# Optimization experiments

Measured on AMD Instinct MI355X. Metric: run time of the kernel, lower is better.

Reference implementation:

```python
import jax, jax.numpy as jnp
import numpy as np

B, N = 8, 64          # batch, keywords per utterance
D = 768               # audio/transformer d_model
T = 512               # CLIP text embedding dim
V = 49408             # CLIP BPE vocab size
TAU = 0.1             # VQ softmax temperature
EPS = 1e-8            # cosine-similarity eps (matches F.cosine_similarity)


def setup_inputs() -> dict:
    key = jax.random.key(0)
    k1, k2, k3 = jax.random.split(key, 3)
    return {
        "audio_feat": jax.random.normal(k1, (B, N, D), dtype=jnp.float32),
        "W_proj": jax.random.normal(k2, (D, T), dtype=jnp.float32) * 0.02,
        "b_proj": jnp.zeros((T,), dtype=jnp.float32),
        "token_emb": jax.random.normal(k3, (V, T), dtype=jnp.float32) * 0.02,
    }


def _l2_normalize(x, axis):
    n = jnp.sqrt(jnp.sum(x * x, axis=axis, keepdims=True))
    return x / jnp.maximum(n, EPS)


def reference(audio_feat, W_proj, b_proj, token_emb):
    # project_feats_to_CLIPspace: linear projection d_model -> text_dim
    kw = jnp.einsum("bnd,dt->bnt", audio_feat, W_proj) + b_proj  # [B,N,T]

    # get_keyword_cosine_score: cosine sim vs full CLIP vocab, expressed as
    # one normalized GEMM instead of the per-keyword broadcast loop.
    kw_n = _l2_normalize(kw, axis=-1)            # [B,N,T]
    emb_n = _l2_normalize(token_emb, axis=-1)    # [V,T]
    cos_score = jnp.einsum("bnt,vt->bnv", kw_n, emb_n)  # [B,N,V]

    # vector quantizer: straight-through hard selection over the vocab
    prob = jax.nn.softmax(cos_score / TAU, axis=-1)              # [B,N,V]
    hard = jax.nn.one_hot(jnp.argmax(cos_score, axis=-1), V,
                          dtype=cos_score.dtype)                  # [B,N,V]
    subword_prob = hard + prob - jax.lax.stop_gradient(prob)

    # keywords = subword_prob @ frozen token embedding table
    keywords = jnp.einsum("bnv,vt->bnt", subword_prob, token_emb)  # [B,N,T]
    return keywords
```

## Files before the change

### kernel.cpp

```cpp
#include <hip/hip_runtime.h>

constexpr int M_ROWS = 512;
constexpr int D_IN   = 768;
constexpr int T_DIM  = 512;
constexpr int V_SIZE = 49408;
constexpr float EPS  = 1e-8f;

typedef short bf16x8 __attribute__((ext_vector_type(8)));
typedef float f32x16 __attribute__((ext_vector_type(16)));

__device__ inline unsigned short bf16_rne(float f) {
  unsigned int u = __float_as_uint(f);
  u += 0x7FFFu + ((u >> 16) & 1u);
  return (unsigned short)(u >> 16);
}
__device__ inline float bf16_f32(unsigned short h) {
  return __uint_as_float(((unsigned int)h) << 16);
}
__device__ inline unsigned int f32_sortable(float f) {
  unsigned int u = __float_as_uint(f);
  return (u & 0x80000000u) ? ~u : (u | 0x80000000u);
}
__device__ inline unsigned long long shfl_xor_u64(unsigned long long x, int mask) {
  unsigned int lo = (unsigned int)(x & 0xFFFFFFFFull);
  unsigned int hi = (unsigned int)(x >> 32);
  lo = __shfl_xor(lo, mask);
  hi = __shfl_xor(hi, mask);
  return ((unsigned long long)hi << 32) | (unsigned long long)lo;
}

__global__ __launch_bounds__(256) void proj_kernel(
    const float* __restrict__ audio, const float* __restrict__ W,
    const float* __restrict__ bias, unsigned short* __restrict__ kwH,
    unsigned short* __restrict__ kwL) {
  __shared__ float a[4][D_IN];
  const int tid = threadIdx.x;
  const int m0 = blockIdx.x * 4;

  const float4* src4 = reinterpret_cast<const float4*>(audio + (size_t)m0 * D_IN);
  float4* a4 = reinterpret_cast<float4*>(&a[0][0]);
  #pragma unroll
  for (int i = 0; i < 3; ++i) a4[tid + 256 * i] = src4[tid + 256 * i];
  __syncthreads();

  const int t0 = tid, t1 = tid + 256;
  float acc[4][2] = {};
  #pragma unroll 4
  for (int d = 0; d < D_IN; ++d) {
    const float w0 = W[(size_t)d * T_DIM + t0];
    const float w1 = W[(size_t)d * T_DIM + t1];
    #pragma unroll
    for (int r = 0; r < 4; ++r) {
      acc[r][0] = fmaf(a[r][d], w0, acc[r][0]);
      acc[r][1] = fmaf(a[r][d], w1, acc[r][1]);
    }
  }
  const float b0 = bias[t0], b1 = bias[t1];
  #pragma unroll
  for (int r = 0; r < 4; ++r) {
    const float v0 = acc[r][0] + b0;
    const float v1 = acc[r][1] + b1;
    const unsigned short h0 = bf16_rne(v0);
    const unsigned short h1 = bf16_rne(v1);
    kwH[(size_t)(m0 + r) * T_DIM + t0] = h0;
    kwH[(size_t)(m0 + r) * T_DIM + t1] = h1;
    kwL[(size_t)(m0 + r) * T_DIM + t0] = bf16_rne(v0 - bf16_f32(h0));
    kwL[(size_t)(m0 + r) * T_DIM + t1] = bf16_rne(v1 - bf16_f32(h1));
  }
}

__global__ __launch_bounds__(256) void norm_kernel(
    const float* __restrict__ emb, float* __restrict__ inv_norm) {
  const int wave = threadIdx.x >> 6;
  const int lane = threadIdx.x & 63;
  const int v = blockIdx.x * 4 + wave;
  const float4* row = reinterpret_cast<const float4*>(emb + (size_t)v * T_DIM);
  const float4 x = row[lane];
  const float4 y = row[lane + 64];
  float ss = x.x * x.x + x.y * x.y + x.z * x.z + x.w * x.w +
             y.x * y.x + y.y * y.y + y.z * y.z + y.w * y.w;
  #pragma unroll
  for (int off = 32; off > 0; off >>= 1) ss += __shfl_xor(ss, off);
  if (lane == 0) inv_norm[v] = 1.0f / fmaxf(sqrtf(ss), EPS);
}

__global__ __launch_bounds__(256, 2) void score_kernel(
    const unsigned short* __restrict__ kwH, const unsigned short* __restrict__ kwL,
    const float* __restrict__ emb, const float* __restrict__ inv_norm,
    unsigned long long* __restrict__ best) {
  __shared__ short ldsH[2][8][64][8];
  __shared__ short ldsL[2][8][64][8];

  const int tid  = threadIdx.x;
  const int lane = tid & 63;
  const int w    = tid >> 6;
  const int n0   = blockIdx.x * 128;
  const int m0   = blockIdx.y * 256;

  size_t sg[2];
  float  ssc[2];
  int    sof[2];
  #pragma unroll
  for (int p = 0; p < 2; ++p) {
    const int s  = tid + 256 * p;
    const int ls = s & 63;
    const int nt = (s >> 6) & 3;
    const int ks = (s >> 8) & 1;
    const int col  = nt * 32 + (ls & 31);
    const int krel = ks * 16 + (ls >> 5) * 8;
    sg[p]  = (size_t)(n0 + col) * T_DIM + krel;
    ssc[p] = inv_norm[n0 + col];
    sof[p] = ((ks * 4 + nt) * 64 + ls) * 8;
  }

  const int kh = (lane >> 5) * 8;
  size_t aOff[2];
  #pragma unroll
  for (int rt = 0; rt < 2; ++rt)
    aOff[rt] = (size_t)(m0 + w * 64 + rt * 32 + (lane & 31)) * T_DIM + kh;

  f32x16 acc[2][4];
  #pragma unroll
  for (int rt = 0; rt < 2; ++rt)
    #pragma unroll
    for (int ct = 0; ct < 4; ++ct)
      #pragma unroll
      for (int i = 0; i < 16; ++i) acc[rt][ct][i] = 0.0f;

  float ld[2][8];

  #pragma unroll
  for (int p = 0; p < 2; ++p) {
    const float4 x0 = *reinterpret_cast<const float4*>(&emb[sg[p]]);
    const float4 x1 = *reinterpret_cast<const float4*>(&emb[sg[p] + 4]);
    ld[p][0] = x0.x; ld[p][1] = x0.y; ld[p][2] = x0.z; ld[p][3] = x0.w;
    ld[p][4] = x1.x; ld[p][5] = x1.y; ld[p][6] = x1.z; ld[p][7] = x1.w;
  }
  {
    short* hw = &ldsH[0][0][0][0];
    short* lw = &ldsL[0][0][0][0];
    #pragma unroll
    for (int p = 0; p < 2; ++p) {
      bf16x8 hv, lv;
      #pragma unroll
      for (int j = 0; j < 8; ++j) {
        const float x = ld[p][j] * ssc[p];
        const unsigned short h = bf16_rne(x);
        hv[j] = (short)h;
        lv[j] = (short)bf16_rne(x - bf16_f32(h));
      }
      *reinterpret_cast<bf16x8*>(hw + sof[p]) = hv;
      *reinterpret_cast<bf16x8*>(lw + sof[p]) = lv;
    }
  }
  __syncthreads();

  for (int ci = 0; ci < 16; ++ci) {
    const int buf = ci & 1;

    if (ci < 15) {
      #pragma unroll
      for (int p = 0; p < 2; ++p) {
        const size_t g = sg[p] + (size_t)(ci + 1) * 32;
        const float4 x0 = *reinterpret_cast<const float4*>(&emb[g]);
        const float4 x1 = *reinterpret_cast<const float4*>(&emb[g + 4]);
        ld[p][0] = x0.x; ld[p][1] = x0.y; ld[p][2] = x0.z; ld[p][3] = x0.w;
        ld[p][4] = x1.x; ld[p][5] = x1.y; ld[p][6] = x1.z; ld[p][7] = x1.w;
      }
    }

    const short* hq = &ldsH[buf][0][0][0];
    const short* lq = &ldsL[buf][0][0][0];
    #pragma unroll
    for (int ks = 0; ks < 2; ++ks) {
      const size_t ak = (size_t)(ci * 32 + ks * 16);
      bf16x8 aH[2], aL[2];
      #pragma unroll
      for (int rt = 0; rt < 2; ++rt) {
        aH[rt] = *reinterpret_cast<const bf16x8*>(&kwH[aOff[rt] + ak]);
        aL[rt] = *reinterpret_cast<const bf16x8*>(&kwL[aOff[rt] + ak]);
      }
      #pragma unroll
      for (int ct = 0; ct < 4; ++ct) {
        const bf16x8 bH = *reinterpret_cast<const bf16x8*>(hq + ((ks * 4 + ct) * 64 + lane) * 8);
        const bf16x8 bL = *reinterpret_cast<const bf16x8*>(lq + ((ks * 4 + ct) * 64 + lane) * 8);
        #pragma unroll
        for (int rt = 0; rt < 2; ++rt) {
          acc[rt][ct] = __builtin_amdgcn_mfma_f32_32x32x16_bf16(aH[rt], bH, acc[rt][ct], 0, 0, 0);
          acc[rt][ct] = __builtin_amdgcn_mfma_f32_32x32x16_bf16(aH[rt], bL, acc[rt][ct], 0, 0, 0);
          acc[rt][ct] = __builtin_amdgcn_mfma_f32_32x32x16_bf16(aL[rt], bH, acc[rt][ct], 0, 0, 0);
        }
      }
    }

    if (ci < 15) {
      short* hw = &ldsH[buf ^ 1][0][0][0];
      short* lw = &ldsL[buf ^ 1][0][0][0];
      #pragma unroll
      for (int p = 0; p < 2; ++p) {
        bf16x8 hv, lv;
        #pragma unroll
        for (int j = 0; j < 8; ++j) {
          const float x = ld[p][j] * ssc[p];
          const unsigned short h = bf16_rne(x);
          hv[j] = (short)h;
          lv[j] = (short)bf16_rne(x - bf16_f32(h));
        }
        *reinterpret_cast<bf16x8*>(hw + sof[p]) = hv;
        *reinterpret_cast<bf16x8*>(lw + sof[p]) = lv;
      }
    }
    __syncthreads();
  }

  #pragma unroll
  for (int rt = 0; rt < 2; ++rt) {
    const int rowbase = m0 + w * 64 + rt * 32 + 4 * (lane >> 5);
    #pragma unroll
    for (int reg = 0; reg < 16; ++reg) {
      const int row = rowbase + (reg & 3) + 8 * (reg >> 2);
      unsigned long long pk = 0;
      #pragma unroll
      for (int ct = 0; ct < 4; ++ct) {
        const float s = acc[rt][ct][reg];
        const unsigned long long p =
            ((unsigned long long)f32_sortable(s) << 32) |
            (unsigned long long)(0xFFFFFFFFu - (unsigned)(n0 + ct * 32 + (lane & 31)));
        if (p > pk) pk = p;
      }
      #pragma unroll
      for (int off = 1; off < 32; off <<= 1) {
        const unsigned long long o = shfl_xor_u64(pk, off);
        if (o > pk) pk = o;
      }
      if ((lane & 31) == 0) atomicMax(&best[row], pk);
    }
  }
}

__global__ __launch_bounds__(128) void gather_kernel(
    const float* __restrict__ emb, const unsigned long long* __restrict__ best,
    float* __restrict__ out) {
  const int row = blockIdx.x;
  const unsigned int idx =
      0xFFFFFFFFu - (unsigned int)(best[row] & 0xFFFFFFFFull);
  const float4* src = reinterpret_cast<const float4*>(emb + (size_t)idx * T_DIM);
  float4* dst = reinterpret_cast<float4*>(out + (size_t)row * T_DIM);
  dst[threadIdx.x] = src[threadIdx.x];
}

extern "C" void kernel_launch(void* const* d_in, const int* in_sizes, int n_in,
                              void* d_out, int out_size, void* d_ws, size_t ws_size,
                              hipStream_t stream) {
  const float* audio = (const float*)d_in[0];
  const float* Wp    = (const float*)d_in[1];
  const float* bp    = (const float*)d_in[2];
  const float* emb   = (const float*)d_in[3];
  float* out = (float*)d_out;

  char* ws = (char*)d_ws;
  unsigned short* kwH = (unsigned short*)ws;
  unsigned short* kwL = kwH + (size_t)M_ROWS * T_DIM;
  float* inv_norm = (float*)(ws + (size_t)2 * M_ROWS * T_DIM * 2);
  unsigned long long* best = (unsigned long long*)(inv_norm + V_SIZE);

  hipMemsetAsync(best, 0, M_ROWS * sizeof(unsigned long long), stream);

  proj_kernel<<<M_ROWS / 4, 256, 0, stream>>>(audio, Wp, bp, kwH, kwL);
  norm_kernel<<<V_SIZE / 4, 256, 0, stream>>>(emb, inv_norm);
  score_kernel<<<dim3(V_SIZE / 128, M_ROWS / 256), 256, 0, stream>>>(
      kwH, kwL, emb, inv_norm, best);
  gather_kernel<<<M_ROWS, 128, 0, stream>>>(emb, best, out);
}
```

Baseline: 383.9 us.

## Pre-split normalized embeddings into MFMA fragment layout before score GEMM

A new split_kernel normalizes each embedding row and writes its bf16 hi/lo parts once, in MFMA fragment-tiled order. The keyword projection output is written in the same fragment order. The score kernel then streams ready-made bf16 fragments, uses 128-row tiles with one row-tile per wave and a higher occupancy bound. Before, every score block re-read fp32 embeddings and redid the scaling and split. The cost is an extra full write and read of the bf16 table (about 100MB of workspace), and the old path stays as a fallback when workspace is too small.

```diff
diff --git a/kernel.cpp b/kernel.cpp
--- a/kernel.cpp
+++ b/kernel.cpp
@@ -4,6 +4,8 @@
 constexpr int D_IN   = 768;
 constexpr int T_DIM  = 512;
 constexpr int V_SIZE = 49408;
+constexpr int NV32   = V_SIZE / 32;
+constexpr int NK16   = T_DIM / 16;
 constexpr float EPS  = 1e-8f;
 
 typedef short bf16x8 __attribute__((ext_vector_type(8)));
@@ -29,6 +31,12 @@
   return ((unsigned long long)hi << 32) | (unsigned long long)lo;
 }
 
+__device__ inline size_t frag_idx(int tile_slot, int rc, int k) {
+  return (size_t)tile_slot * 512 +
+         (size_t)(((rc & 31) | (((k >> 3) & 1) << 5)) * 8) + (k & 7);
+}
+
+template <int FRAG>
 __global__ __launch_bounds__(256) void proj_kernel(
     const float* __restrict__ audio, const float* __restrict__ W,
     const float* __restrict__ bias, unsigned short* __restrict__ kwH,
@@ -58,14 +66,178 @@
   const float b0 = bias[t0], b1 = bias[t1];
   #pragma unroll
   for (int r = 0; r < 4; ++r) {
+    const int row = m0 + r;
     const float v0 = acc[r][0] + b0;
     const float v1 = acc[r][1] + b1;
     const unsigned short h0 = bf16_rne(v0);
     const unsigned short h1 = bf16_rne(v1);
-    kwH[(size_t)(m0 + r) * T_DIM + t0] = h0;
-    kwH[(size_t)(m0 + r) * T_DIM + t1] = h1;
-    kwL[(size_t)(m0 + r) * T_DIM + t0] = bf16_rne(v0 - bf16_f32(h0));
-    kwL[(size_t)(m0 + r) * T_DIM + t1] = bf16_rne(v1 - bf16_f32(h1));
+    const unsigned short l0 = bf16_rne(v0 - bf16_f32(h0));
+    const unsigned short l1 = bf16_rne(v1 - bf16_f32(h1));
+    if (FRAG) {
+      const size_t i0 = frag_idx((row >> 5) * NK16 + (t0 >> 4), row, t0);
+      const size_t i1 = frag_idx((row >> 5) * NK16 + (t1 >> 4), row, t1);
+      kwH[i0] = h0; kwH[i1] = h1;
+      kwL[i0] = l0; kwL[i1] = l1;
+    } else {
+      kwH[(size_t)row * T_DIM + t0] = h0;
+      kwH[(size_t)row * T_DIM + t1] = h1;
+      kwL[(size_t)row * T_DIM + t0] = l0;
+      kwL[(size_t)row * T_DIM + t1] = l1;
+    }
+  }
+}
+
+__global__ __launch_bounds__(256) void split_kernel(
+    const float* __restrict__ emb, unsigned short* __restrict__ embHf,
+    unsigned short* __restrict__ embLf) {
+  __shared__ float lds_inv[32];
+  const int tid = threadIdx.x;
+  const int v0 = blockIdx.x * 32;
+
+  {
+    const float* rp = emb + (size_t)(v0 + (tid >> 3)) * T_DIM + (tid & 7) * 64;
+    const float4* rp4 = reinterpret_cast<const float4*>(rp);
+    float ss = 0.0f;
+    #pragma unroll
+    for (int i = 0; i < 16; ++i) {
+      const float4 x = rp4[i];
+      ss += x.x * x.x + x.y * x.y + x.z * x.z + x.w * x.w;
+    }
+    ss += __shfl_xor(ss, 1);
+    ss += __shfl_xor(ss, 2);
+    ss += __shfl_xor(ss, 4);
+    if ((tid & 7) == 0) lds_inv[tid >> 3] = 1.0f / fmaxf(sqrtf(ss), EPS);
+  }
+  __syncthreads();
+
+  const int w = tid >> 6, l = tid & 63;
+  const float s = lds_inv[l & 31];
+  const size_t gbase = (size_t)(v0 + (l & 31)) * T_DIM + (l >> 5) * 8;
+  const size_t obase = (size_t)blockIdx.x * 32 * 512 + (size_t)l * 8;
+  #pragma unroll
+  for (int i = 0; i < 8; ++i) {
+    const int k16 = w * 8 + i;
+    const float4 x0 = *reinterpret_cast<const float4*>(&emb[gbase + k16 * 16]);
+    const float4 x1 = *reinterpret_cast<const float4*>(&emb[gbase + k16 * 16 + 4]);
+    const float xv[8] = {x0.x, x0.y, x0.z, x0.w, x1.x, x1.y, x1.z, x1.w};
+    bf16x8 hv, lv;
+    #pragma unroll
+    for (int j = 0; j < 8; ++j) {
+      const float x = xv[j] * s;
+      const unsigned short h = bf16_rne(x);
+      hv[j] = (short)h;
+      lv[j] = (short)bf16_rne(x - bf16_f32(h));
+    }
+    *reinterpret_cast<bf16x8*>(&embHf[obase + (size_t)k16 * 512]) = hv;
+    *reinterpret_cast<bf16x8*>(&embLf[obase + (size_t)k16 * 512]) = lv;
+  }
+}
+
+__global__ __launch_bounds__(256, 4) void score_kernel(
+    const unsigned short* __restrict__ kwHf, const unsigned short* __restrict__ kwLf,
+    const unsigned short* __restrict__ embHf, const unsigned short* __restrict__ embLf,
+    unsigned long long* __restrict__ best) {
+  __shared__ short ldsB[2][2][4][2][512];
+
+  const int tid  = threadIdx.x;
+  const int lane = tid & 63;
+  const int w    = tid >> 6;
+  const int xb   = blockIdx.x;
+  const int m0   = blockIdx.y * 128;
+
+  const unsigned short* gp[4];
+  int ldsOff[4];
+  #pragma unroll
+  for (int q = 0; q < 4; ++q) {
+    const int idx = w * 4 + q;
+    const int hl = idx & 1, k16o = (idx >> 1) & 1, v32o = idx >> 2;
+    const unsigned short* src = hl ? embLf : embHf;
+    gp[q] = src + ((size_t)(xb * 4 + v32o) * NK16 + k16o) * 512 + (size_t)lane * 8;
+    ldsOff[q] = ((k16o * 4 + v32o) * 2 + hl) * 512 + lane * 8;
+  }
+
+  const unsigned short* aHp =
+      kwHf + (size_t)((m0 >> 5) + w) * NK16 * 512 + (size_t)lane * 8;
+  const unsigned short* aLp =
+      kwLf + (size_t)((m0 >> 5) + w) * NK16 * 512 + (size_t)lane * 8;
+
+  f32x16 acc[4];
+  #pragma unroll
+  for (int ct = 0; ct < 4; ++ct)
+    #pragma unroll
+    for (int i = 0; i < 16; ++i) acc[ct][i] = 0.0f;
+
+  bf16x8 sreg[4];
+
+  #pragma unroll
+  for (int q = 0; q < 4; ++q) sreg[q] = *reinterpret_cast<const bf16x8*>(gp[q]);
+  {
+    short* b0 = &ldsB[0][0][0][0][0];
+    #pragma unroll
+    for (int q = 0; q < 4; ++q)
+      *reinterpret_cast<bf16x8*>(b0 + ldsOff[q]) = sreg[q];
+  }
+  __syncthreads();
+
+  for (int ci = 0; ci < 16; ++ci) {
+    const int buf = ci & 1;
+
+    if (ci < 15) {
+      #pragma unroll
+      for (int q = 0; q < 4; ++q)
+        sreg[q] = *reinterpret_cast<const bf16x8*>(gp[q] + (size_t)(ci + 1) * 1024);
+    }
+
+    bf16x8 aH[2], aL[2];
+    #pragma unroll
+    for (int ks = 0; ks < 2; ++ks) {
+      aH[ks] = *reinterpret_cast<const bf16x8*>(aHp + (size_t)(ci * 2 + ks) * 512);
+      aL[ks] = *reinterpret_cast<const bf16x8*>(aLp + (size_t)(ci * 2 + ks) * 512);
+    }
+
+    const short* bb = &ldsB[buf][0][0][0][0];
+    #pragma unroll
+    for (int ks = 0; ks < 2; ++ks) {
+      #pragma unroll
+      for (int ct = 0; ct < 4; ++ct) {
+        const bf16x8 bH = *reinterpret_cast<const bf16x8*>(
+            bb + ((ks * 4 + ct) * 2 + 0) * 512 + lane * 8);
+        const bf16x8 bL = *reinterpret_cast<const bf16x8*>(
+            bb + ((ks * 4 + ct) * 2 + 1) * 512 + lane * 8);
+        acc[ct] = __builtin_amdgcn_mfma_f32_32x32x16_bf16(aH[ks], bH, acc[ct], 0, 0, 0);
+        acc[ct] = __builtin_amdgcn_mfma_f32_32x32x16_bf16(aH[ks], bL, acc[ct], 0, 0, 0);
+        acc[ct] = __builtin_amdgcn_mfma_f32_32x32x16_bf16(aL[ks], bH, acc[ct], 0, 0, 0);
+      }
+    }
+
+    if (ci < 15) {
+      short* bn = &ldsB[buf ^ 1][0][0][0][0];
+      #pragma unroll
+      for (int q = 0; q < 4; ++q)
+        *reinterpret_cast<bf16x8*>(bn + ldsOff[q]) = sreg[q];
+    }
+    __syncthreads();
+  }
+
+  const int rowbase = m0 + w * 32 + 4 * (lane >> 5);
+  #pragma unroll
+  for (int reg = 0; reg < 16; ++reg) {
+    const int row = rowbase + (reg & 3) + 8 * (reg >> 2);
+    unsigned long long pk = 0;
+    #pragma unroll
+    for (int ct = 0; ct < 4; ++ct) {
+      const float s = acc[ct][reg];
+      const unsigned long long p =
+          ((unsigned long long)f32_sortable(s) << 32) |
+          (unsigned long long)(0xFFFFFFFFu - (unsigned)(xb * 128 + ct * 32 + (lane & 31)));
+      if (p > pk) pk = p;
+    }
+    #pragma unroll
+    for (int off = 1; off < 32; off <<= 1) {
+      const unsigned long long o = shfl_xor_u64(pk, off);
+      if (o > pk) pk = o;
+    }
+    if ((lane & 31) == 0) atomicMax(&best[row], pk);
   }
 }
 
@@ -84,22 +256,18 @@
   if (lane == 0) inv_norm[v] = 1.0f / fmaxf(sqrtf(ss), EPS);
 }
 
-__global__ __launch_bounds__(256, 2) void score_kernel(
+__global__ __launch_bounds__(256, 2) void score_v1_kernel(
     const unsigned short* __restrict__ kwH, const unsigned short* __restrict__ kwL,
     const float* __restrict__ emb, const float* __restrict__ inv_norm,
     unsigned long long* __restrict__ best) {
   __shared__ short ldsH[2][8][64][8];
   __shared__ short ldsL[2][8][64][8];
-
   const int tid  = threadIdx.x;
   const int lane = tid & 63;
   const int w    = tid >> 6;
   const int n0   = blockIdx.x * 128;
   const int m0   = blockIdx.y * 256;
-
-  size_t sg[2];
-  float  ssc[2];
-  int    sof[2];
+  size_t sg[2]; float ssc[2]; int sof[2];
   #pragma unroll
   for (int p = 0; p < 2; ++p) {
     const int s  = tid + 256 * p;
@@ -112,13 +280,11 @@
     ssc[p] = inv_norm[n0 + col];
     sof[p] = ((ks * 4 + nt) * 64 + ls) * 8;
   }
-
   const int kh = (lane >> 5) * 8;
   size_t aOff[2];
   #pragma unroll
   for (int rt = 0; rt < 2; ++rt)
     aOff[rt] = (size_t)(m0 + w * 64 + rt * 32 + (lane & 31)) * T_DIM + kh;
-
   f32x16 acc[2][4];
   #pragma unroll
   for (int rt = 0; rt < 2; ++rt)
@@ -126,9 +292,7 @@
     for (int ct = 0; ct < 4; ++ct)
       #pragma unroll
       for (int i = 0; i < 16; ++i) acc[rt][ct][i] = 0.0f;
-
   float ld[2][8];
-
   #pragma unroll
   for (int p = 0; p < 2; ++p) {
     const float4 x0 = *reinterpret_cast<const float4*>(&emb[sg[p]]);
@@ -154,10 +318,8 @@
     }
   }
   __syncthreads();
-
   for (int ci = 0; ci < 16; ++ci) {
     const int buf = ci & 1;
-
     if (ci < 15) {
       #pragma unroll
       for (int p = 0; p < 2; ++p) {
@@ -168,7 +330,6 @@
         ld[p][4] = x1.x; ld[p][5] = x1.y; ld[p][6] = x1.z; ld[p][7] = x1.w;
       }
     }
-
     const short* hq = &ldsH[buf][0][0][0];
     const short* lq = &ldsL[buf][0][0][0];
     #pragma unroll
@@ -192,7 +353,6 @@
         }
       }
     }
-
     if (ci < 15) {
       short* hw = &ldsH[buf ^ 1][0][0][0];
       short* lw = &ldsL[buf ^ 1][0][0][0];
@@ -212,7 +372,6 @@
     }
     __syncthreads();
   }
-
   #pragma unroll
   for (int rt = 0; rt < 2; ++rt) {
     const int rowbase = m0 + w * 64 + rt * 32 + 4 * (lane >> 5);
@@ -258,17 +417,36 @@
   const float* emb   = (const float*)d_in[3];
   float* out = (float*)d_out;
 
+  const size_t kw_elems  = (size_t)M_ROWS * T_DIM;
+  const size_t emb_elems = (size_t)V_SIZE * T_DIM;
+  const size_t need = 2 * kw_elems * 2 + 2 * emb_elems * 2 +
+                      M_ROWS * sizeof(unsigned long long);
+
   char* ws = (char*)d_ws;
-  unsigned short* kwH = (unsigned short*)ws;
-  unsigned short* kwL = kwH + (size_t)M_ROWS * T_DIM;
-  float* inv_norm = (float*)(ws + (size_t)2 * M_ROWS * T_DIM * 2);
-  unsigned long long* best = (unsigned long long*)(inv_norm + V_SIZE);
-
-  hipMemsetAsync(best, 0, M_ROWS * sizeof(unsigned long long), stream);
-
-  proj_kernel<<<M_ROWS / 4, 256, 0, stream>>>(audio, Wp, bp, kwH, kwL);
-  norm_kernel<<<V_SIZE / 4, 256, 0, stream>>>(emb, inv_norm);
-  score_kernel<<<dim3(V_SIZE / 128, M_ROWS / 256), 256, 0, stream>>>(
-      kwH, kwL, emb, inv_norm, best);
-  gather_kernel<<<M_ROWS, 128, 0, stream>>>(emb, best, out);
-}
+  if (ws_size >= need) {
+    unsigned short* kwHf  = (unsigned short*)ws;
+    unsigned short* kwLf  = kwHf + kw_elems;
+    unsigned short* embHf = kwLf + kw_elems;
+    unsigned short* embLf = embHf + emb_elems;
+    unsigned long long* best = (unsigned long long*)(embLf + emb_elems);
+
+    hipMemsetAsync(best, 0, M_ROWS * sizeof(unsigned long long), stream);
+    proj_kernel<1><<<M_ROWS / 4, 256, 0, stream>>>(audio, Wp, bp, kwHf, kwLf);
+    split_kernel<<<NV32, 256, 0, stream>>>(emb, embHf, embLf);
+    score_kernel<<<dim3(V_SIZE / 128, M_ROWS / 128), 256, 0, stream>>>(
+        kwHf, kwLf, embHf, embLf, best);
+    gather_kernel<<<M_ROWS, 128, 0, stream>>>(emb, best, out);
+  } else {
+    unsigned short* kwH = (unsigned short*)ws;
+    unsigned short* kwL = kwH + kw_elems;
+    float* inv_norm = (float*)(kwL + kw_elems);
+    unsigned long long* best = (unsigned long long*)(inv_norm + V_SIZE);
+
+    hipMemsetAsync(best, 0, M_ROWS * sizeof(unsigned long long), stream);
+    proj_kernel<0><<<M_ROWS / 4, 256, 0, stream>>>(audio, Wp, bp, kwH, kwL);
+    norm_kernel<<<V_SIZE / 4, 256, 0, stream>>>(emb, inv_norm);
+    score_v1_kernel<<<dim3(V_SIZE / 128, M_ROWS / 256), 256, 0, stream>>>(
+        kwH, kwL, emb, inv_norm, best);
+    gather_kernel<<<M_ROWS, 128, 0, stream>>>(emb, best, out);
+  }
+}
```

Result: slower. 403.7 us (+5.2%).

## Fuse vocab norm into score kernel, retile to all rows per block with fragment layout

Applied to the files above, without the earlier changes.

Removes the separate norm kernel by accumulating sum of squares of each vocab row while it is loaded, then applies the inverse norm to the accumulated scores before the argmax. Each block now covers all 512 query rows against 64 vocab rows, so the embedding table is read once instead of twice. The projected keywords are stored in a pre-swizzled MFMA fragment layout for contiguous loads. Because raw rather than normalized embeddings are split into bf16 hi/lo, precision changes slightly, and each block now does more work with fewer blocks in the grid.

```diff
diff --git a/kernel.cpp b/kernel.cpp
--- a/kernel.cpp
+++ b/kernel.cpp
@@ -4,6 +4,7 @@
 constexpr int D_IN   = 768;
 constexpr int T_DIM  = 512;
 constexpr int V_SIZE = 49408;
+constexpr int NK16   = T_DIM / 16;
 constexpr float EPS  = 1e-8f;
 
 typedef short bf16x8 __attribute__((ext_vector_type(8)));
@@ -27,6 +28,11 @@
   lo = __shfl_xor(lo, mask);
   hi = __shfl_xor(hi, mask);
   return ((unsigned long long)hi << 32) | (unsigned long long)lo;
+}
+
+__device__ inline size_t frag_idx(int tile_slot, int rc, int k) {
+  return (size_t)tile_slot * 512 +
+         (size_t)(((rc & 31) | (((k >> 3) & 1) << 5)) * 8) + (k & 7);
 }
 
 __global__ __launch_bounds__(256) void proj_kernel(
@@ -58,100 +64,74 @@
   const float b0 = bias[t0], b1 = bias[t1];
   #pragma unroll
   for (int r = 0; r < 4; ++r) {
+    const int row = m0 + r;
     const float v0 = acc[r][0] + b0;
     const float v1 = acc[r][1] + b1;
     const unsigned short h0 = bf16_rne(v0);
     const unsigned short h1 = bf16_rne(v1);
-    kwH[(size_t)(m0 + r) * T_DIM + t0] = h0;
-    kwH[(size_t)(m0 + r) * T_DIM + t1] = h1;
-    kwL[(size_t)(m0 + r) * T_DIM + t0] = bf16_rne(v0 - bf16_f32(h0));
-    kwL[(size_t)(m0 + r) * T_DIM + t1] = bf16_rne(v1 - bf16_f32(h1));
-  }
-}
-
-__global__ __launch_bounds__(256) void norm_kernel(
-    const float* __restrict__ emb, float* __restrict__ inv_norm) {
-  const int wave = threadIdx.x >> 6;
-  const int lane = threadIdx.x & 63;
-  const int v = blockIdx.x * 4 + wave;
-  const float4* row = reinterpret_cast<const float4*>(emb + (size_t)v * T_DIM);
-  const float4 x = row[lane];
-  const float4 y = row[lane + 64];
-  float ss = x.x * x.x + x.y * x.y + x.z * x.z + x.w * x.w +
-             y.x * y.x + y.y * y.y + y.z * y.z + y.w * y.w;
-  #pragma unroll
-  for (int off = 32; off > 0; off >>= 1) ss += __shfl_xor(ss, off);
-  if (lane == 0) inv_norm[v] = 1.0f / fmaxf(sqrtf(ss), EPS);
+    const size_t i0 = frag_idx((row >> 5) * NK16 + (t0 >> 4), row, t0);
+    const size_t i1 = frag_idx((row >> 5) * NK16 + (t1 >> 4), row, t1);
+    kwH[i0] = h0; kwH[i1] = h1;
+    kwL[i0] = bf16_rne(v0 - bf16_f32(h0));
+    kwL[i1] = bf16_rne(v1 - bf16_f32(h1));
+  }
 }
 
 __global__ __launch_bounds__(256, 2) void score_kernel(
-    const unsigned short* __restrict__ kwH, const unsigned short* __restrict__ kwL,
-    const float* __restrict__ emb, const float* __restrict__ inv_norm,
-    unsigned long long* __restrict__ best) {
-  __shared__ short ldsH[2][8][64][8];
-  __shared__ short ldsL[2][8][64][8];
+    const unsigned short* __restrict__ kwHf, const unsigned short* __restrict__ kwLf,
+    const float* __restrict__ emb, unsigned long long* __restrict__ best) {
+  __shared__ short ldsB[2][8][512];
+  __shared__ float lds_ss[4][32];
 
   const int tid  = threadIdx.x;
   const int lane = tid & 63;
   const int w    = tid >> 6;
-  const int n0   = blockIdx.x * 128;
-  const int m0   = blockIdx.y * 256;
-
-  size_t sg[2];
-  float  ssc[2];
-  int    sof[2];
-  #pragma unroll
-  for (int p = 0; p < 2; ++p) {
-    const int s  = tid + 256 * p;
-    const int ls = s & 63;
-    const int nt = (s >> 6) & 3;
-    const int ks = (s >> 8) & 1;
-    const int col  = nt * 32 + (ls & 31);
-    const int krel = ks * 16 + (ls >> 5) * 8;
-    sg[p]  = (size_t)(n0 + col) * T_DIM + krel;
-    ssc[p] = inv_norm[n0 + col];
-    sof[p] = ((ks * 4 + nt) * 64 + ls) * 8;
-  }
-
-  const int kh = (lane >> 5) * 8;
-  size_t aOff[2];
-  #pragma unroll
-  for (int rt = 0; rt < 2; ++rt)
-    aOff[rt] = (size_t)(m0 + w * 64 + rt * 32 + (lane & 31)) * T_DIM + kh;
-
-  f32x16 acc[2][4];
-  #pragma unroll
-  for (int rt = 0; rt < 2; ++rt)
-    #pragma unroll
-    for (int ct = 0; ct < 4; ++ct)
+  const int vb   = blockIdx.x;
+
+  const int col5  = tid & 31;
+  const int khalf = (tid >> 5) & 1;
+  const int k16o  = (tid >> 6) & 1;
+  const int v32o  = tid >> 7;
+  const float* gp =
+      emb + (size_t)(vb * 64 + v32o * 32 + col5) * T_DIM + k16o * 16 + khalf * 8;
+  const int wrOff = ((k16o * 2 + v32o) * 2) * 512 + ((col5 | (khalf << 5)) * 8);
+
+  const unsigned short* aHp[4];
+  const unsigned short* aLp[4];
+  #pragma unroll
+  for (int rt = 0; rt < 4; ++rt) {
+    const size_t base = (size_t)(w * 4 + rt) * NK16 * 512 + (size_t)lane * 8;
+    aHp[rt] = kwHf + base;
+    aLp[rt] = kwLf + base;
+  }
+
+  f32x16 acc[4][2];
+  #pragma unroll
+  for (int rt = 0; rt < 4; ++rt)
+    #pragma unroll
+    for (int ct = 0; ct < 2; ++ct)
       #pragma unroll
       for (int i = 0; i < 16; ++i) acc[rt][ct][i] = 0.0f;
 
-  float ld[2][8];
-
-  #pragma unroll
-  for (int p = 0; p < 2; ++p) {
-    const float4 x0 = *reinterpret_cast<const float4*>(&emb[sg[p]]);
-    const float4 x1 = *reinterpret_cast<const float4*>(&emb[sg[p] + 4]);
-    ld[p][0] = x0.x; ld[p][1] = x0.y; ld[p][2] = x0.z; ld[p][3] = x0.w;
-    ld[p][4] = x1.x; ld[p][5] = x1.y; ld[p][6] = x1.z; ld[p][7] = x1.w;
-  }
+  float ss = 0.0f;
+  float4 x0, x1;
+
+  x0 = *reinterpret_cast<const float4*>(gp);
+  x1 = *reinterpret_cast<const float4*>(gp + 4);
   {
-    short* hw = &ldsH[0][0][0][0];
-    short* lw = &ldsL[0][0][0][0];
-    #pragma unroll
-    for (int p = 0; p < 2; ++p) {
-      bf16x8 hv, lv;
-      #pragma unroll
-      for (int j = 0; j < 8; ++j) {
-        const float x = ld[p][j] * ssc[p];
-        const unsigned short h = bf16_rne(x);
-        hv[j] = (short)h;
-        lv[j] = (short)bf16_rne(x - bf16_f32(h));
-      }
-      *reinterpret_cast<bf16x8*>(hw + sof[p]) = hv;
-      *reinterpret_cast<bf16x8*>(lw + sof[p]) = lv;
-    }
+    ss += x0.x * x0.x + x0.y * x0.y + x0.z * x0.z + x0.w * x0.w +
+          x1.x * x1.x + x1.y * x1.y + x1.z * x1.z + x1.w * x1.w;
+    const float xv[8] = {x0.x, x0.y, x0.z, x0.w, x1.x, x1.y, x1.z, x1.w};
+    bf16x8 hv, lv;
+    #pragma unroll
+    for (int j = 0; j < 8; ++j) {
+      const unsigned short h = bf16_rne(xv[j]);
+      hv[j] = (short)h;
+      lv[j] = (short)bf16_rne(xv[j] - bf16_f32(h));
+    }
+    short* b0 = &ldsB[0][0][0];
+    *reinterpret_cast<bf16x8*>(b0 + wrOff) = hv;
+    *reinterpret_cast<bf16x8*>(b0 + wrOff + 512) = lv;
   }
   __syncthreads();
 
@@ -159,33 +139,27 @@
     const int buf = ci & 1;
 
     if (ci < 15) {
-      #pragma unroll
-      for (int p = 0; p < 2; ++p) {
-        const size_t g = sg[p] + (size_t)(ci + 1) * 32;
-        const float4 x0 = *reinterpret_cast<const float4*>(&emb[g]);
-        const float4 x1 = *reinterpret_cast<const float4*>(&emb[g + 4]);
-        ld[p][0] = x0.x; ld[p][1] = x0.y; ld[p][2] = x0.z; ld[p][3] = x0.w;
-        ld[p][4] = x1.x; ld[p][5] = x1.y; ld[p][6] = x1.z; ld[p][7] = x1.w;
-      }
-    }
-
-    const short* hq = &ldsH[buf][0][0][0];
-    const short* lq = &ldsL[buf][0][0][0];
+      x0 = *reinterpret_cast<const float4*>(gp + (ci + 1) * 32);
+      x1 = *reinterpret_cast<const float4*>(gp + (ci + 1) * 32 + 4);
+    }
+
+    const short* bb = &ldsB[buf][0][0];
     #pragma unroll
     for (int ks = 0; ks < 2; ++ks) {
-      const size_t ak = (size_t)(ci * 32 + ks * 16);
-      bf16x8 aH[2], aL[2];
-      #pragma unroll
-      for (int rt = 0; rt < 2; ++rt) {
-        aH[rt] = *reinterpret_cast<const bf16x8*>(&kwH[aOff[rt] + ak]);
-        aL[rt] = *reinterpret_cast<const bf16x8*>(&kwL[aOff[rt] + ak]);
-      }
-      #pragma unroll
-      for (int ct = 0; ct < 4; ++ct) {
-        const bf16x8 bH = *reinterpret_cast<const bf16x8*>(hq + ((ks * 4 + ct) * 64 + lane) * 8);
-        const bf16x8 bL = *reinterpret_cast<const bf16x8*>(lq + ((ks * 4 + ct) * 64 + lane) * 8);
+      bf16x8 aH[4], aL[4];
+      #pragma unroll
+      for (int rt = 0; rt < 4; ++rt) {
+        aH[rt] = *reinterpret_cast<const bf16x8*>(aHp[rt] + (size_t)(ci * 2 + ks) * 512);
+        aL[rt] = *reinterpret_cast<const bf16x8*>(aLp[rt] + (size_t)(ci * 2 + ks) * 512);
+      }
+      #pragma unroll
+      for (int ct = 0; ct < 2; ++ct) {
+        const bf16x8 bH = *reinterpret_cast<const bf16x8*>(
+            bb + ((ks * 2 + ct) * 2 + 0) * 512 + lane * 8);
+        const bf16x8 bL = *reinterpret_cast<const bf16x8*>(
+            bb + ((ks * 2 + ct) * 2 + 1) * 512 + lane * 8);
         #pragma unroll
-        for (int rt = 0; rt < 2; ++rt) {
+        for (int rt = 0; rt < 4; ++rt) {
           acc[rt][ct] = __builtin_amdgcn_mfma_f32_32x32x16_bf16(aH[rt], bH, acc[rt][ct], 0, 0, 0);
           acc[rt][ct] = __builtin_amdgcn_mfma_f32_32x32x16_bf16(aH[rt], bL, acc[rt][ct], 0, 0, 0);
           acc[rt][ct] = __builtin_amdgcn_mfma_f32_32x32x16_bf16(aL[rt], bH, acc[rt][ct], 0, 0, 0);
@@ -194,38 +168,48 @@
     }
 
     if (ci < 15) {
-      short* hw = &ldsH[buf ^ 1][0][0][0];
-      short* lw = &ldsL[buf ^ 1][0][0][0];
-      #pragma unroll
-      for (int p = 0; p < 2; ++p) {
-        bf16x8 hv, lv;
-        #pragma unroll
-        for (int j = 0; j < 8; ++j) {
-          const float x = ld[p][j] * ssc[p];
-          const unsigned short h = bf16_rne(x);
-          hv[j] = (short)h;
-          lv[j] = (short)bf16_rne(x - bf16_f32(h));
-        }
-        *reinterpret_cast<bf16x8*>(hw + sof[p]) = hv;
-        *reinterpret_cast<bf16x8*>(lw + sof[p]) = lv;
-      }
+      ss += x0.x * x0.x + x0.y * x0.y + x0.z * x0.z + x0.w * x0.w +
+            x1.x * x1.x + x1.y * x1.y + x1.z * x1.z + x1.w * x1.w;
+      const float xv[8] = {x0.x, x0.y, x0.z, x0.w, x1.x, x1.y, x1.z, x1.w};
+      bf16x8 hv, lv;
+      #pragma unroll
+      for (int j = 0; j < 8; ++j) {
+        const unsigned short h = bf16_rne(xv[j]);
+        hv[j] = (short)h;
+        lv[j] = (short)bf16_rne(xv[j] - bf16_f32(h));
+      }
+      short* bn = &ldsB[buf ^ 1][0][0];
+      *reinterpret_cast<bf16x8*>(bn + wrOff) = hv;
+      *reinterpret_cast<bf16x8*>(bn + wrOff + 512) = lv;
     }
     __syncthreads();
   }
 
-  #pragma unroll
-  for (int rt = 0; rt < 2; ++rt) {
-    const int rowbase = m0 + w * 64 + rt * 32 + 4 * (lane >> 5);
+  ss += __shfl_xor(ss, 32);
+  if (lane < 32) lds_ss[w][lane] = ss;
+  __syncthreads();
+
+  const int c5 = lane & 31;
+  float inv[2];
+  #pragma unroll
+  for (int ct = 0; ct < 2; ++ct) {
+    const float sst = lds_ss[ct * 2][c5] + lds_ss[ct * 2 + 1][c5];
+    inv[ct] = 1.0f / fmaxf(sqrtf(sst), EPS);
+  }
+
+  #pragma unroll
+  for (int rt = 0; rt < 4; ++rt) {
+    const int rowbase = w * 128 + rt * 32 + 4 * (lane >> 5);
     #pragma unroll
     for (int reg = 0; reg < 16; ++reg) {
       const int row = rowbase + (reg & 3) + 8 * (reg >> 2);
       unsigned long long pk = 0;
       #pragma unroll
-      for (int ct = 0; ct < 4; ++ct) {
-        const float s = acc[rt][ct][reg];
+      for (int ct = 0; ct < 2; ++ct) {
+        const float s = acc[rt][ct][reg] * inv[ct];
         const unsigned long long p =
             ((unsigned long long)f32_sortable(s) << 32) |
-            (unsigned long long)(0xFFFFFFFFu - (unsigned)(n0 + ct * 32 + (lane & 31)));
+            (unsigned long long)(0xFFFFFFFFu - (unsigned)(vb * 64 + ct * 32 + c5));
         if (p > pk) pk = p;
       }
       #pragma unroll
@@ -233,7 +217,7 @@
         const unsigned long long o = shfl_xor_u64(pk, off);
         if (o > pk) pk = o;
       }
-      if ((lane & 31) == 0) atomicMax(&best[row], pk);
+      if (c5 == 0) atomicMax(&best[row], pk);
     }
   }
 }
@@ -258,17 +242,15 @@
   const float* emb   = (const float*)d_in[3];
   float* out = (float*)d_out;
 
+  const size_t kw_elems = (size_t)M_ROWS * T_DIM;
   char* ws = (char*)d_ws;
-  unsigned short* kwH = (unsigned short*)ws;
-  unsigned short* kwL = kwH + (size_t)M_ROWS * T_DIM;
-  float* inv_norm = (float*)(ws + (size_t)2 * M_ROWS * T_DIM * 2);
-  unsigned long long* best = (unsigned long long*)(inv_norm + V_SIZE);
+  unsigned short* kwHf = (unsigned short*)ws;
+  unsigned short* kwLf = kwHf + kw_elems;
+  unsigned long long* best = (unsigned long long*)(kwLf + kw_elems);
 
   hipMemsetAsync(best, 0, M_ROWS * sizeof(unsigned long long), stream);
 
-  proj_kernel<<<M_ROWS / 4, 256, 0, stream>>>(audio, Wp, bp, kwH, kwL);
-  norm_kernel<<<V_SIZE / 4, 256, 0, stream>>>(emb, inv_norm);
-  score_kernel<<<dim3(V_SIZE / 128, M_ROWS / 256), 256, 0, stream>>>(
-      kwH, kwL, emb, inv_norm, best);
+  proj_kernel<<<M_ROWS / 4, 256, 0, stream>>>(audio, Wp, bp, kwHf, kwLf);
+  score_kernel<<<V_SIZE / 64, 256, 0, stream>>>(kwHf, kwLf, emb, best);
   gather_kernel<<<M_ROWS, 128, 0, stream>>>(emb, best, out);
 }
```

New measurement: 372.2 us. 3.1% less time.
